# Optimization experiments

Hardware: AMD Instinct MI355X
Metric: run time of the kernel (lower is better)

The kernel has to match this reference:

```python
import jax, jax.numpy as jnp
import numpy as np

B, H, L, DK, DV = 8, 8, 1024, 64, 64
N = B * H
TEMP = 8.0  # sqrt(d_k)
A_MIX, B_MIX, C_MIX = 0.1, 0.4, 0.1


def setup_inputs() -> dict:
    key = jax.random.key(0)
    ks = jax.random.split(key, 6)
    q = jax.random.normal(ks[0], (N, L, DK), jnp.float32)
    k = jax.random.normal(ks[1], (N, L, DK), jnp.float32)
    v = jax.random.normal(ks[2], (N, L, DV), jnp.float32)
    q_rm = jax.random.normal(ks[3], (N, L, DK), jnp.float32)
    attn_pre = jax.random.normal(ks[4], (N, L, L), jnp.float32)
    conv_w = jax.random.normal(ks[5], (H, H, 3, 3), jnp.float32) * 0.05  # OIHW, no bias
    # causal mask: True where masked (j > i), broadcast over N
    mask = jnp.broadcast_to(jnp.triu(jnp.ones((L, L), bool), 1), (N, L, L))
    return {"q": q, "k": k, "v": v, "q_rm": q_rm, "attn_pre": attn_pre,
            "conv_w": conv_w, "mask": mask, "fg": 1}


def sift_down_right(src, filled):
    # R[..,1:,1:] = src[..,:-1,:-1]; R[..,0,:] = filled[..,0,:]; R[..,:,0] = filled[..,:,0]
    top = filled[:, 0:1, :]                    # [N,1,L]
    left = filled[:, 1:, 0:1]                  # [N,L-1,1]
    body = jnp.concatenate([left, src[:, :-1, :-1]], axis=-1)  # [N,L-1,L]
    return jnp.concatenate([top, body], axis=1)


def sift_down(src, filled):
    top = filled[:, 0:1, :]
    return jnp.concatenate([top, src[:, :-1, :]], axis=1)


def reference(q, k, v, q_rm, attn_pre, conv_w, mask, fg):
    attn = jnp.einsum('nqd,nkd->nqk', q, k) / TEMP
    attn_rm = jnp.einsum('nqd,nkd->nqk', q_rm, k) / TEMP
    # conv refinement of masked attn_rm, per (batch, head) grid
    x = jnp.where(mask, 0.0, attn_rm).reshape(-1, H, L, L)  # [B,H,L,L]
    x = jax.lax.conv_general_dilated(x, conv_w, (1, 1), 'SAME',
                                     dimension_numbers=('NCHW', 'OIHW', 'NCHW'))
    x = jax.nn.relu(x).reshape(-1, L, L)
    attn_cnn = sift_down_right(x, attn_rm) if fg == 1 else sift_down(x, attn_rm)
    attn_cnn = attn_cnn * C_MIX + attn_rm * (1.0 - C_MIX)
    attn = attn_cnn * B_MIX + attn * (1.0 - B_MIX)
    attn = attn_pre * A_MIX + attn * (1.0 - A_MIX)
    attn = jnp.where(mask, -jnp.inf, attn)
    attn = jax.nn.softmax(attn, axis=-1)
    # dropout is identity in eval/deterministic baseline
    out = jnp.einsum('nqk,nkd->nqd', attn, v)
    return out, attn
```

## Files before the change

kernel.cpp:

```cpp
#include <hip/hip_runtime.h>
#include <cstdint>
#include <cstddef>
#include <math.h>

#define L_ 1024
#define DK_ 64
#define DV_ 64
#define N_ 64
#define H_ 8
#define B_ 8

__global__ __launch_bounds__(256) void k1_qk_tril(
    const float* __restrict__ qrm, const float* __restrict__ kk,
    float* __restrict__ xm) {
  const int n  = blockIdx.z;
  const int q0 = blockIdx.y * 64;
  const int j0 = blockIdx.x * 64;
  const int t  = threadIdx.x;

  if (j0 > q0) {
    const float4 z = make_float4(0.f, 0.f, 0.f, 0.f);
    #pragma unroll
    for (int i = 0; i < 4; ++i) {
      const int row = (t >> 4) + i * 16;
      const int c4  = t & 15;
      float4* p = (float4*)(xm + ((size_t)(n * L_ + q0 + row)) * L_ + j0);
      p[c4] = z;
    }
    return;
  }

  __shared__ float As[64][65];
  __shared__ float Bs[64][65];
  #pragma unroll
  for (int i = 0; i < 4; ++i) {
    const int row = (t >> 4) + i * 16;
    const int c4  = t & 15;
    const float4 a = ((const float4*)(qrm + ((size_t)(n * L_ + q0 + row)) * DK_))[c4];
    const float4 b = ((const float4*)(kk  + ((size_t)(n * L_ + j0 + row)) * DK_))[c4];
    As[row][c4 * 4 + 0] = a.x; As[row][c4 * 4 + 1] = a.y;
    As[row][c4 * 4 + 2] = a.z; As[row][c4 * 4 + 3] = a.w;
    Bs[row][c4 * 4 + 0] = b.x; Bs[row][c4 * 4 + 1] = b.y;
    Bs[row][c4 * 4 + 2] = b.z; Bs[row][c4 * 4 + 3] = b.w;
  }
  __syncthreads();

  const int ty = t >> 4, tx = t & 15;
  float acc[4][4];
  #pragma unroll
  for (int i = 0; i < 4; ++i)
    #pragma unroll
    for (int j = 0; j < 4; ++j) acc[i][j] = 0.f;

  for (int d = 0; d < 64; ++d) {
    float a[4], b[4];
    #pragma unroll
    for (int i = 0; i < 4; ++i) a[i] = As[ty * 4 + i][d];
    #pragma unroll
    for (int j = 0; j < 4; ++j) b[j] = Bs[tx * 4 + j][d];
    #pragma unroll
    for (int i = 0; i < 4; ++i)
      #pragma unroll
      for (int j = 0; j < 4; ++j) acc[i][j] += a[i] * b[j];
  }

  #pragma unroll
  for (int i = 0; i < 4; ++i) {
    const int gq = q0 + ty * 4 + i;
    float* rowp = xm + ((size_t)(n * L_ + gq)) * L_;
    #pragma unroll
    for (int j = 0; j < 4; ++j) {
      const int gj = j0 + tx * 4 + j;
      rowp[gj] = (gj <= gq) ? acc[i][j] * 0.125f : 0.f;
    }
  }
}

__global__ __launch_bounds__(256) void k2_conv(
    const float* __restrict__ xm, const float* __restrict__ w,
    float* __restrict__ xs) {
  const int ct = blockIdx.x, rt = blockIdx.y, b = blockIdx.z;
  const int r0 = rt * 4, c0 = ct * 64;
  if (c0 > r0 + 4) return;

  __shared__ float in_s[8][6][68];
  __shared__ float ws[576];
  const int t = threadIdx.x;

  for (int i = t; i < 576; i += 256) ws[i] = w[i];
  for (int e = t; e < 8 * 6 * 66; e += 256) {
    const int hi  = e / 396;
    const int rem = e - hi * 396;
    const int rr  = rem / 66;
    const int cc  = rem - rr * 66;
    const int gr  = r0 - 1 + rr;
    const int gc  = c0 - 1 + cc;
    float v = 0.f;
    if (gr >= 0 && gr < L_ && gc >= 0 && gc < L_)
      v = xm[((size_t)((b * 8 + hi) * L_ + gr)) * L_ + gc];
    in_s[hi][rr][cc] = v;
  }
  __syncthreads();

  const int cc = t & 63;
  const int rr = t >> 6;
  float acc[8];
  #pragma unroll
  for (int ho = 0; ho < 8; ++ho) acc[ho] = 0.f;

  #pragma unroll
  for (int hi = 0; hi < 8; ++hi) {
    float iv[3][3];
    #pragma unroll
    for (int di = 0; di < 3; ++di)
      #pragma unroll
      for (int dj = 0; dj < 3; ++dj)
        iv[di][dj] = in_s[hi][rr + di][cc + dj];
    #pragma unroll
    for (int ho = 0; ho < 8; ++ho) {
      const float* wp = &ws[(ho * 8 + hi) * 9];
      #pragma unroll
      for (int di = 0; di < 3; ++di)
        #pragma unroll
        for (int dj = 0; dj < 3; ++dj)
          acc[ho] += iv[di][dj] * wp[di * 3 + dj];
    }
  }

  const int gr = r0 + rr, gc = c0 + cc;
  #pragma unroll
  for (int ho = 0; ho < 8; ++ho)
    xs[((size_t)((b * 8 + ho) * L_ + gr)) * L_ + gc] = fmaxf(acc[ho], 0.f);
}

__global__ __launch_bounds__(256) void k3_fused(
    const float* __restrict__ q, const float* __restrict__ kk,
    const float* __restrict__ v, const float* __restrict__ pre,
    const int* __restrict__ fgp, const float* __restrict__ xs,
    float* attn, float* __restrict__ out) {
  const int bid  = blockIdx.y * gridDim.x + blockIdx.x;
  const int work = (bid & 7) * 512 + (bid >> 3);
  const int n    = work >> 6;
  const int q0   = (63 - (work & 63)) * 16;

  const int t    = threadIdx.x;
  const int lane = t & 63;
  const int g    = t >> 6;
  const int fg   = *fgp;

  const int srow = t >> 4;
  const int c4   = t & 15;

  __shared__ float tiles[2][64][64];
  __shared__ float qps[2][16][64];

  int r_[4], lr_[4];
  #pragma unroll
  for (int i = 0; i < 4; ++i) { r_[i] = q0 + g + i * 4; lr_[i] = g + i * 4; }
  size_t rowoff[4];
  #pragma unroll
  for (int i = 0; i < 4; ++i) rowoff[i] = ((size_t)(n * L_ + r_[i])) * L_;

  const int ntiles = (q0 >> 6) + 1;
  const float* kbase = kk + (size_t)n * L_ * DK_;
  const int wswz = (c4 ^ srow) << 2;
  const int lx = lane & 15;

  {
    const float4 qx =
        *(const float4*)(q + ((size_t)(n * L_ + q0 + srow)) * DK_ + c4 * 4);
    *(float4*)&qps[0][srow][c4 * 4] = qx;
  }
  #pragma unroll
  for (int i = 0; i < 4; ++i) {
    const int row = srow + i * 16;
    const float4 kx = *(const float4*)(kbase + (size_t)row * DK_ + c4 * 4);
    *(float4*)&tiles[0][row][wswz] = kx;
  }
  __syncthreads();

  float m[4], l[4];
  #pragma unroll
  for (int i = 0; i < 4; ++i) { m[i] = -1e30f; l[i] = 0.f; }

  for (int tile = 0; tile < ntiles; ++tile) {
    const int cur = tile & 1, nxt = cur ^ 1;
    const int j0 = tile * 64;
    const int j  = j0 + lane;
    const bool havenext = (tile + 1) < ntiles;

    float4 kpre[4];
    if (havenext) {
      const float* kb2 = kbase + (size_t)(j0 + 64) * DK_;
      #pragma unroll
      for (int i = 0; i < 4; ++i)
        kpre[i] = *(const float4*)(kb2 + (size_t)(srow + i * 16) * DK_ + c4 * 4);
    }

    float rmv[4], prv[4], xsv[4];
    #pragma unroll
    for (int i = 0; i < 4; ++i) {
      const int r = r_[i];
      const bool act = (j <= r);
      rmv[i] = act ? attn[rowoff[i] + j] : 0.f;
      prv[i] = act ? pre[rowoff[i] + j] : 0.f;
      if (fg == 1)
        xsv[i] = (act && r > 0 && j > 0)
                     ? xs[rowoff[i] - L_ + (j - 1)] : 0.f;
      else
        xsv[i] = (act && r > 0) ? xs[rowoff[i] - L_ + j] : 0.f;
    }

    float dot[4] = {0.f, 0.f, 0.f, 0.f};
    const float* krow = &tiles[cur][0][0] + lane * 64;
    #pragma unroll 4
    for (int gg = 0; gg < 16; ++gg) {
      const float4 kq = *(const float4*)(krow + ((gg ^ lx) << 2));
      #pragma unroll
      for (int i = 0; i < 4; ++i) {
        const float4 q4 = *(const float4*)&qps[0][lr_[i]][gg << 2];
        dot[i] += q4.x * kq.x + q4.y * kq.y + q4.z * kq.z + q4.w * kq.w;
      }
    }

    #pragma unroll
    for (int i = 0; i < 4; ++i) {
      const int r = r_[i];
      float s = -INFINITY;
      if (j <= r) {
        const float sqk = dot[i] * 0.125f;
        const float cnn = (fg == 1)
                              ? ((r == 0 || j == 0) ? rmv[i] : xsv[i])
                              : ((r == 0) ? rmv[i] : xsv[i]);
        const float mixed = cnn * 0.1f + rmv[i] * 0.9f;
        const float a2    = mixed * 0.4f + sqk * 0.6f;
        s = prv[i] * 0.1f + a2 * 0.9f;
      }
      attn[rowoff[i] + j] = s;

      const float mn = fmaxf(m[i], s);
      l[i] = l[i] * __expf(m[i] - mn) + __expf(s - mn);
      m[i] = mn;
    }

    if (havenext) {
      #pragma unroll
      for (int i = 0; i < 4; ++i) {
        const int row = srow + i * 16;
        *(float4*)&tiles[nxt][row][wswz] = kpre[i];
      }
    }
    __syncthreads();
  }

  #pragma unroll
  for (int i = 0; i < 4; ++i) {
    float mf = m[i];
    #pragma unroll
    for (int o = 32; o > 0; o >>= 1) mf = fmaxf(mf, __shfl_xor(mf, o));
    float ls = l[i] * __expf(m[i] - mf);
    #pragma unroll
    for (int o = 32; o > 0; o >>= 1) ls += __shfl_xor(ls, o);
    m[i] = mf;
    l[i] = ls;
  }

  float invl[4];
  #pragma unroll
  for (int i = 0; i < 4; ++i) invl[i] = 1.f / l[i];

  float acc[4] = {0.f, 0.f, 0.f, 0.f};
  const float* vb = v + (size_t)n * L_ * DV_;

  #pragma unroll
  for (int i = 0; i < 4; ++i) {
    const int row = srow + i * 16;
    const float4 vx = *(const float4*)(vb + (size_t)row * DV_ + c4 * 4);
    *(float4*)&tiles[0][row][c4 * 4] = vx;
  }
  #pragma unroll
  for (int i = 0; i < 4; ++i) {
    const float s  = attn[rowoff[i] + lane];
    const float pv = __expf(s - m[i]) * invl[i];
    qps[0][lr_[i]][lane] = pv;
    attn[rowoff[i] + lane] = pv;
  }
  __syncthreads();

  for (int tile = 0; tile < ntiles; ++tile) {
    const int cur = tile & 1, nxt = cur ^ 1;
    const int j0 = tile * 64;
    const bool havenext = (tile + 1) < ntiles;

    float4 vpre[4];
    float s_nxt[4];
    if (havenext) {
      const float* vb2 = vb + (size_t)(j0 + 64) * DV_;
      #pragma unroll
      for (int i = 0; i < 4; ++i)
        vpre[i] = *(const float4*)(vb2 + (size_t)(srow + i * 16) * DV_ + c4 * 4);
      #pragma unroll
      for (int i = 0; i < 4; ++i)
        s_nxt[i] = attn[rowoff[i] + j0 + 64 + lane];
    }

    #pragma unroll 4
    for (int cs = 0; cs < 16; ++cs) {
      const int c0 = cs * 4;
      const float v0 = tiles[cur][c0 + 0][lane];
      const float v1 = tiles[cur][c0 + 1][lane];
      const float v2 = tiles[cur][c0 + 2][lane];
      const float v3 = tiles[cur][c0 + 3][lane];
      #pragma unroll
      for (int i = 0; i < 4; ++i) {
        const float4 pr = *(const float4*)&qps[cur][lr_[i]][c0];
        acc[i] += pr.x * v0 + pr.y * v1 + pr.z * v2 + pr.w * v3;
      }
    }

    if (havenext) {
      #pragma unroll
      for (int i = 0; i < 4; ++i) {
        const int row = srow + i * 16;
        *(float4*)&tiles[nxt][row][c4 * 4] = vpre[i];
      }
      #pragma unroll
      for (int i = 0; i < 4; ++i) {
        const float pv = __expf(s_nxt[i] - m[i]) * invl[i];
        qps[nxt][lr_[i]][lane] = pv;
        attn[rowoff[i] + j0 + 64 + lane] = pv;
      }
    }
    __syncthreads();
  }

  #pragma unroll
  for (int i = 0; i < 4; ++i)
    out[((size_t)(n * L_ + r_[i])) * DV_ + lane] = acc[i];
}

extern "C" void kernel_launch(void* const* d_in, const int* in_sizes, int n_in,
                              void* d_out, int out_size, void* d_ws,
                              size_t ws_size, hipStream_t stream) {
  const float* q   = (const float*)d_in[0];
  const float* kk  = (const float*)d_in[1];
  const float* v   = (const float*)d_in[2];
  const float* qrm = (const float*)d_in[3];
  const float* pre = (const float*)d_in[4];
  const float* cw  = (const float*)d_in[5];
  const int* fg = (const int*)d_in[7];

  float* out  = (float*)d_out;
  float* attn = out + (size_t)N_ * L_ * DV_;
  float* xs   = (float*)d_ws;

  k1_qk_tril<<<dim3(16, 16, 64), 256, 0, stream>>>(qrm, kk, attn);
  k2_conv<<<dim3(16, 256, 8), 256, 0, stream>>>(attn, cw, xs);
  k3_fused<<<dim3(64, 64), 256, 0, stream>>>(q, kk, v, pre, fg, xs, attn, out);
}
```

Before: 1.474 ms.

## Enlarge QK tile to 128x128, vectorize conv halo loads, reverse PV tile order

The QK^T masked kernel moves to 128x128 tiles with 8x8 per-thread accumulators and float4 shared-memory loads, which raises arithmetic intensity and cuts shared-memory traffic. The conv kernel's halo load becomes aligned float4 global loads with a wider padded shared buffer, replacing scalar loads that used divisions. The fused softmax/PV kernel walks key tiles from last to first, likely so the most recently written attn data is still cache-resident. The larger tiles raise register pressure and coarsen diagonal-tile work, which may reduce occupancy.

```diff
diff --git a/kernel.cpp b/kernel.cpp
--- a/kernel.cpp
+++ b/kernel.cpp
@@ -14,64 +14,67 @@
     const float* __restrict__ qrm, const float* __restrict__ kk,
     float* __restrict__ xm) {
   const int n  = blockIdx.z;
-  const int q0 = blockIdx.y * 64;
-  const int j0 = blockIdx.x * 64;
+  const int by = blockIdx.y, bx = blockIdx.x;
+  const int q0 = by * 128, j0 = bx * 128;
   const int t  = threadIdx.x;
 
-  if (j0 > q0) {
+  if (bx > by) {
     const float4 z = make_float4(0.f, 0.f, 0.f, 0.f);
     #pragma unroll
-    for (int i = 0; i < 4; ++i) {
-      const int row = (t >> 4) + i * 16;
-      const int c4  = t & 15;
-      float4* p = (float4*)(xm + ((size_t)(n * L_ + q0 + row)) * L_ + j0);
-      p[c4] = z;
+    for (int i = 0; i < 16; ++i) {
+      const int idx = t + i * 256;
+      const int row = idx >> 5, c4 = idx & 31;
+      *(float4*)(xm + ((size_t)(n * L_ + q0 + row)) * L_ + j0 + c4 * 4) = z;
     }
     return;
   }
 
-  __shared__ float As[64][65];
-  __shared__ float Bs[64][65];
-  #pragma unroll
-  for (int i = 0; i < 4; ++i) {
-    const int row = (t >> 4) + i * 16;
-    const int c4  = t & 15;
-    const float4 a = ((const float4*)(qrm + ((size_t)(n * L_ + q0 + row)) * DK_))[c4];
-    const float4 b = ((const float4*)(kk  + ((size_t)(n * L_ + j0 + row)) * DK_))[c4];
-    As[row][c4 * 4 + 0] = a.x; As[row][c4 * 4 + 1] = a.y;
-    As[row][c4 * 4 + 2] = a.z; As[row][c4 * 4 + 3] = a.w;
-    Bs[row][c4 * 4 + 0] = b.x; Bs[row][c4 * 4 + 1] = b.y;
-    Bs[row][c4 * 4 + 2] = b.z; Bs[row][c4 * 4 + 3] = b.w;
+  __shared__ float As[128][68];
+  __shared__ float Bs[128][68];
+  #pragma unroll
+  for (int i = 0; i < 8; ++i) {
+    const int idx = t + i * 256;
+    const int row = idx >> 4, c4 = idx & 15;
+    *(float4*)&As[row][c4 * 4] =
+        *(const float4*)(qrm + ((size_t)(n * L_ + q0 + row)) * DK_ + c4 * 4);
+    *(float4*)&Bs[row][c4 * 4] =
+        *(const float4*)(kk + ((size_t)(n * L_ + j0 + row)) * DK_ + c4 * 4);
   }
   __syncthreads();
 
-  const int ty = t >> 4, tx = t & 15;
-  float acc[4][4];
-  #pragma unroll
-  for (int i = 0; i < 4; ++i)
-    #pragma unroll
-    for (int j = 0; j < 4; ++j) acc[i][j] = 0.f;
-
-  for (int d = 0; d < 64; ++d) {
-    float a[4], b[4];
-    #pragma unroll
-    for (int i = 0; i < 4; ++i) a[i] = As[ty * 4 + i][d];
-    #pragma unroll
-    for (int j = 0; j < 4; ++j) b[j] = Bs[tx * 4 + j][d];
-    #pragma unroll
-    for (int i = 0; i < 4; ++i)
-      #pragma unroll
-      for (int j = 0; j < 4; ++j) acc[i][j] += a[i] * b[j];
-  }
-
-  #pragma unroll
-  for (int i = 0; i < 4; ++i) {
-    const int gq = q0 + ty * 4 + i;
+  const int ty16 = t >> 4;
+  const int tx   = t & 15;
+
+  float acc[8][8];
+  #pragma unroll
+  for (int ii = 0; ii < 8; ++ii)
+    #pragma unroll
+    for (int jj = 0; jj < 8; ++jj) acc[ii][jj] = 0.f;
+
+  #pragma unroll 2
+  for (int d0 = 0; d0 < 64; d0 += 4) {
+    float4 b4[8];
+    #pragma unroll
+    for (int jj = 0; jj < 8; ++jj)
+      b4[jj] = *(const float4*)&Bs[tx + 16 * jj][d0];
+    #pragma unroll
+    for (int ii = 0; ii < 8; ++ii) {
+      const float4 a4 = *(const float4*)&As[ty16 + 16 * ii][d0];
+      #pragma unroll
+      for (int jj = 0; jj < 8; ++jj)
+        acc[ii][jj] += a4.x * b4[jj].x + a4.y * b4[jj].y +
+                       a4.z * b4[jj].z + a4.w * b4[jj].w;
+    }
+  }
+
+  #pragma unroll
+  for (int ii = 0; ii < 8; ++ii) {
+    const int gq = q0 + ty16 + 16 * ii;
     float* rowp = xm + ((size_t)(n * L_ + gq)) * L_;
     #pragma unroll
-    for (int j = 0; j < 4; ++j) {
-      const int gj = j0 + tx * 4 + j;
-      rowp[gj] = (gj <= gq) ? acc[i][j] * 0.125f : 0.f;
+    for (int jj = 0; jj < 8; ++jj) {
+      const int gj = j0 + tx + 16 * jj;
+      rowp[gj] = (gj <= gq) ? acc[ii][jj] * 0.125f : 0.f;
     }
   }
 }
@@ -83,22 +86,27 @@
   const int r0 = rt * 4, c0 = ct * 64;
   if (c0 > r0 + 4) return;
 
-  __shared__ float in_s[8][6][68];
+  __shared__ float in_s[8][6][76];
   __shared__ float ws[576];
   const int t = threadIdx.x;
 
   for (int i = t; i < 576; i += 256) ws[i] = w[i];
-  for (int e = t; e < 8 * 6 * 66; e += 256) {
-    const int hi  = e / 396;
-    const int rem = e - hi * 396;
-    const int rr  = rem / 66;
-    const int cc  = rem - rr * 66;
-    const int gr  = r0 - 1 + rr;
-    const int gc  = c0 - 1 + cc;
-    float v = 0.f;
-    if (gr >= 0 && gr < L_ && gc >= 0 && gc < L_)
-      v = xm[((size_t)((b * 8 + hi) * L_ + gr)) * L_ + gc];
-    in_s[hi][rr][cc] = v;
+
+  #pragma unroll
+  for (int i = 0; i < 4; ++i) {
+    const int e = t + i * 256;
+    if (e < 864) {
+      const int ch  = e / 108;
+      const int rem = e - ch * 108;
+      const int row = rem / 18;
+      const int f4  = rem - row * 18;
+      const int gr  = r0 - 1 + row;
+      const int gc  = c0 - 4 + f4 * 4;
+      float4 val = make_float4(0.f, 0.f, 0.f, 0.f);
+      if (gr >= 0 && gr < L_ && gc >= 0 && gc <= L_ - 4)
+        val = *(const float4*)(xm + ((size_t)((b * 8 + ch) * L_ + gr)) * L_ + gc);
+      *(float4*)&in_s[ch][row][f4 * 4] = val;
+    }
   }
   __syncthreads();
 
@@ -115,7 +123,7 @@
     for (int di = 0; di < 3; ++di)
       #pragma unroll
       for (int dj = 0; dj < 3; ++dj)
-        iv[di][dj] = in_s[hi][rr + di][cc + dj];
+        iv[di][dj] = in_s[hi][rr + di][cc + 3 + dj];
     #pragma unroll
     for (int ho = 0; ho < 8; ++ho) {
       const float* wp = &ws[(ho * 8 + hi) * 9];
@@ -271,37 +279,39 @@
 
   float acc[4] = {0.f, 0.f, 0.f, 0.f};
   const float* vb = v + (size_t)n * L_ * DV_;
+  const int jlast = (ntiles - 1) * 64;
 
   #pragma unroll
   for (int i = 0; i < 4; ++i) {
     const int row = srow + i * 16;
-    const float4 vx = *(const float4*)(vb + (size_t)row * DV_ + c4 * 4);
+    const float4 vx =
+        *(const float4*)(vb + (size_t)(jlast + row) * DV_ + c4 * 4);
     *(float4*)&tiles[0][row][c4 * 4] = vx;
   }
   #pragma unroll
   for (int i = 0; i < 4; ++i) {
-    const float s  = attn[rowoff[i] + lane];
+    const float s  = attn[rowoff[i] + jlast + lane];
     const float pv = __expf(s - m[i]) * invl[i];
     qps[0][lr_[i]][lane] = pv;
-    attn[rowoff[i] + lane] = pv;
+    attn[rowoff[i] + jlast + lane] = pv;
   }
   __syncthreads();
 
-  for (int tile = 0; tile < ntiles; ++tile) {
-    const int cur = tile & 1, nxt = cur ^ 1;
-    const int j0 = tile * 64;
-    const bool havenext = (tile + 1) < ntiles;
+  for (int it = 0; it < ntiles; ++it) {
+    const int cur = it & 1, nxt = cur ^ 1;
+    const int j0 = (ntiles - 1 - it) * 64;
+    const bool havenext = (it + 1) < ntiles;
 
     float4 vpre[4];
     float s_nxt[4];
     if (havenext) {
-      const float* vb2 = vb + (size_t)(j0 + 64) * DV_;
+      const float* vb2 = vb + (size_t)(j0 - 64) * DV_;
       #pragma unroll
       for (int i = 0; i < 4; ++i)
         vpre[i] = *(const float4*)(vb2 + (size_t)(srow + i * 16) * DV_ + c4 * 4);
       #pragma unroll
       for (int i = 0; i < 4; ++i)
-        s_nxt[i] = attn[rowoff[i] + j0 + 64 + lane];
+        s_nxt[i] = attn[rowoff[i] + j0 - 64 + lane];
     }
 
     #pragma unroll 4
@@ -328,7 +338,7 @@
       for (int i = 0; i < 4; ++i) {
         const float pv = __expf(s_nxt[i] - m[i]) * invl[i];
         qps[nxt][lr_[i]][lane] = pv;
-        attn[rowoff[i] + j0 + 64 + lane] = pv;
+        attn[rowoff[i] + j0 - 64 + lane] = pv;
       }
     }
     __syncthreads();
@@ -354,7 +364,7 @@
   float* attn = out + (size_t)N_ * L_ * DV_;
   float* xs   = (float*)d_ws;
 
-  k1_qk_tril<<<dim3(16, 16, 64), 256, 0, stream>>>(qrm, kk, attn);
+  k1_qk_tril<<<dim3(8, 8, 64), 256, 0, stream>>>(qrm, kk, attn);
   k2_conv<<<dim3(16, 256, 8), 256, 0, stream>>>(attn, cw, xs);
   k3_fused<<<dim3(64, 64), 256, 0, stream>>>(q, kk, v, pre, fg, xs, attn, out);
 }
```

Result: faster. 1.444 ms (-2.0%).
